# Optimization experiments

Hardware: AMD Instinct MI355X
Metric: run time of the kernel (lower is better)

The kernel has to match this reference:

```python
import jax, jax.numpy as jnp
import numpy as np

EPS = 1e-5

def knn_idx(x, k):
    # x: (B,C,N). Returns (B,N,k) indices of k nearest neighbors (by L2).
    inner = -2.0 * jnp.einsum('bcn,bcm->bnm', x, x)          # (B,N,N)
    xx = jnp.sum(x * x, axis=1)                               # (B,N)
    neg_dist = -xx[:, :, None] - inner - xx[:, None, :]       # (B,N,N)
    _, idx = jax.lax.top_k(neg_dist, k)                       # (B,N,k)
    return idx

def get_graph_features(x, k):
    # x: (B,C,N) -> (B,2C,N,k) with channels = concat(neighbor-center, center)
    B, C, N = x.shape
    idx = knn_idx(x, k)                                       # (B,N,k)
    pts = jnp.transpose(x, (0, 2, 1))                         # (B,N,C)
    nbr = jax.vmap(lambda p, i: p[i])(pts, idx)               # (B,N,k,C)
    ctr = jnp.broadcast_to(pts[:, :, None, :], nbr.shape)     # (B,N,k,C)
    feat = jnp.concatenate([nbr - ctr, ctr], axis=-1)         # (B,N,k,2C)
    return jnp.transpose(feat, (0, 3, 1, 2))                  # (B,2C,N,k)

def conv_bn_relu(y, W, gamma, beta):
    # 1x1 conv (pointwise matmul) + train-mode BatchNorm2d + ReLU
    y = jnp.einsum('oc,bcnk->bonk', W, y)
    mean = jnp.mean(y, axis=(0, 2, 3), keepdims=True)
    var = jnp.var(y, axis=(0, 2, 3), keepdims=True)
    yhat = (y - mean) * jax.lax.rsqrt(var + EPS)
    return jax.nn.relu(yhat * gamma[None, :, None, None] + beta[None, :, None, None])

def setup_inputs() -> dict:
    key = jax.random.key(0)
    ks = jax.random.split(key, 16)
    B, N, k, emb = 8, 2048, 20, 512
    x = jax.random.normal(ks[0], (B, 3, N), dtype=jnp.float32)
    def w(kk, o, c):
        return jax.random.normal(kk, (o, c), dtype=jnp.float32) * (1.0 / np.sqrt(c))
    inp = {
        'x': x, 'k': k,
        'W1': w(ks[1], 64, 6),   'W2': w(ks[2], 64, 64),
        'W3': w(ks[3], 128, 64), 'W4': w(ks[4], 256, 128),
        'W5': w(ks[5], emb, 512),
    }
    for i, c in zip(range(1, 6), [64, 64, 128, 256, emb]):
        inp[f'g{i}'] = 1.0 + 0.1 * jax.random.normal(ks[5 + i], (c,), dtype=jnp.float32)
        inp[f'b{i}'] = 0.1 * jax.random.normal(ks[10 + i], (c,), dtype=jnp.float32)
    return inp

def reference(x, W1, W2, W3, W4, W5, g1, b1, g2, b2, g3, b3, g4, b4, g5, b5, k):
    B, C, N = x.shape
    h = get_graph_features(x, k)                  # (B,6,N,k)
    h = conv_bn_relu(h, W1, g1, b1)               # (B,64,N,k)
    x1 = jnp.max(h, axis=-1, keepdims=True)
    h = conv_bn_relu(h, W2, g2, b2)               # (B,64,N,k)
    x2 = jnp.max(h, axis=-1, keepdims=True)
    h = conv_bn_relu(h, W3, g3, b3)               # (B,128,N,k)
    x3 = jnp.max(h, axis=-1, keepdims=True)
    h = conv_bn_relu(h, W4, g4, b4)               # (B,256,N,k)
    x4 = jnp.max(h, axis=-1, keepdims=True)
    cat = jnp.concatenate([x1, x2, x3, x4], axis=1)  # (B,512,N,1)
    out = conv_bn_relu(cat, W5, g5, b5)              # (B,emb,N,1)
    return out.reshape(B, -1, N)
```

## Files before the change

### kernel.cpp

```cpp
#include <hip/hip_runtime.h>
#include <hip/hip_bf16.h>

typedef __hip_bfloat16 bf16;
typedef __attribute__((ext_vector_type(8))) short short8v;
typedef __attribute__((ext_vector_type(4))) float f32x4;
typedef unsigned int uint;

#define BATCH 8
#define NPTS 2048
#define KNN 20
#define NK (NPTS*KNN)
#define P4 (BATCH*NK)
#define BN_TOT (BATCH*NPTS)

union BU { bf16 h; unsigned short u; };
__device__ __forceinline__ unsigned short f2bf(float f){
    BU bu; bu.h = __float2bfloat16(f); return bu.u;
}
__device__ __forceinline__ float bfu2f(unsigned short u){
    return __uint_as_float(((uint)u) << 16);
}

__global__ void initK(float* __restrict__ shadow)
{
    int t = blockIdx.x*256 + threadIdx.x;
    if (t < 5*16*1024) shadow[t] = 0.f;
}

__global__ void cvtWS(const float* __restrict__ src, short* __restrict__ dst, int Cin)
{
    int t = blockIdx.x*256 + threadIdx.x;
    int co = t / Cin, ci = t - co*Cin;
    dst[(size_t)co*Cin + (ci ^ ((co & 7) << 3))] = (short)f2bf(src[t]);
}

__global__ __launch_bounds__(256)
void knn_kernel(const float* __restrict__ x, int* __restrict__ idx)
{
    #pragma clang fp contract(off)
    __shared__ float sx[3*NPTS];
    __shared__ float sxx[NPTS];
    const int b  = blockIdx.x / (NPTS/4);
    const int nb = blockIdx.x % (NPTS/4);
    const float* xb = x + (size_t)b*3*NPTS;
    for (int i = threadIdx.x; i < 3*NPTS; i += 256) sx[i] = xb[i];
    __syncthreads();
    for (int i = threadIdx.x; i < NPTS; i += 256) {
        float y0 = sx[i], y1 = sx[NPTS+i], y2 = sx[2*NPTS+i];
        sxx[i] = y0*y0 + y1*y1 + y2*y2;
    }
    __syncthreads();

    const int wave = threadIdx.x >> 6;
    const int lane = threadIdx.x & 63;
    const int n = nb*4 + wave;

    const float x0 = sx[n], x1 = sx[NPTS+n], x2 = sx[2*NPTS+n];
    const float xxn = sxx[n];

    constexpr int L = 6;
    float best[L]; int bi[L];
    #pragma unroll
    for (int i = 0; i < L; ++i) { best[i] = -3e38f; bi[i] = 0x7fffffff; }

    #pragma unroll
    for (int j = 0; j < NPTS/64; ++j) {
        int m = lane + j*64;
        float dot = x0*sx[m] + x1*sx[NPTS+m] + x2*sx[2*NPTS+m];
        float v = -xxn - (-2.f*dot) - sxx[m];
        int mi = m;
        #pragma unroll
        for (int i = 0; i < L; ++i) {
            bool sw = v > best[i];
            float tv = sw ? best[i] : v;
            int   ti = sw ? bi[i]   : mi;
            best[i] = sw ? v  : best[i];
            bi[i]   = sw ? mi : bi[i];
            v = tv; mi = ti;
        }
    }

    size_t obase = ((size_t)b*NPTS + n)*KNN;
    int popped = 0;
    #pragma unroll 1
    for (int s = 0; s < KNN; ++s) {
        float mv = best[0]; int mi = bi[0];
        #pragma unroll
        for (int off = 1; off < 64; off <<= 1) {
            float ov = __shfl_xor(mv, off);
            int   oi = __shfl_xor(mi, off);
            if (ov > mv || (ov == mv && oi < mi)) { mv = ov; mi = oi; }
        }
        bool win = (best[0] == mv) && (bi[0] == mi);
        #pragma unroll
        for (int i = 0; i < L-1; ++i) {
            best[i] = win ? best[i+1] : best[i];
            bi[i]   = win ? bi[i+1]   : bi[i];
        }
        best[L-1] = win ? -3e38f     : best[L-1];
        bi[L-1]   = win ? 0x7fffffff : bi[L-1];
        popped += win ? 1 : 0;
        if (lane == 0) idx[obase + s] = mi;
    }

    if (__any(popped >= L)) {
        float B[KNN]; int BI[KNN];
        #pragma unroll
        for (int i = 0; i < KNN; ++i) { B[i] = -3e38f; BI[i] = 0x7fffffff; }
        #pragma unroll 1
        for (int j = 0; j < NPTS/64; ++j) {
            int m = lane + j*64;
            float dot = x0*sx[m] + x1*sx[NPTS+m] + x2*sx[2*NPTS+m];
            float v = -xxn - (-2.f*dot) - sxx[m];
            int mi = m;
            #pragma unroll
            for (int i = 0; i < KNN; ++i) {
                bool sw = v > B[i];
                float tv = sw ? B[i]  : v;
                int   ti = sw ? BI[i] : mi;
                B[i]  = sw ? v  : B[i];
                BI[i] = sw ? mi : BI[i];
                v = tv; mi = ti;
            }
        }
        #pragma unroll 1
        for (int s = 0; s < KNN; ++s) {
            float mv = B[0]; int mi = BI[0];
            #pragma unroll
            for (int off = 1; off < 64; off <<= 1) {
                float ov = __shfl_xor(mv, off);
                int   oi = __shfl_xor(mi, off);
                if (ov > mv || (ov == mv && oi < mi)) { mv = ov; mi = oi; }
            }
            bool win = (B[0] == mv) && (BI[0] == mi);
            #pragma unroll
            for (int i = 0; i < KNN-1; ++i) {
                B[i]  = win ? B[i+1]  : B[i];
                BI[i] = win ? BI[i+1] : BI[i];
            }
            B[KNN-1]  = win ? -3e38f     : B[KNN-1];
            BI[KNN-1] = win ? 0x7fffffff : BI[KNN-1];
            if (lane == 0) idx[obase + s] = mi;
        }
    }
}

__global__ void conv1T(const float* __restrict__ x, const int* __restrict__ idx,
                       const float* __restrict__ W1, bf16* __restrict__ h1)
{
    int p = blockIdx.x*256 + threadIdx.x;
    int b = p / NK;
    int r = p - b*NK;
    int n = r / KNN;
    int j = idx[p];
    const float* xb = x + (size_t)b*3*NPTS;
    float c0 = xb[n], c1 = xb[NPTS+n], c2 = xb[2*NPTS+n];
    float d0 = xb[j]-c0, d1 = xb[NPTS+j]-c1, d2 = xb[2*NPTS+j]-c2;
    uint4* outp = reinterpret_cast<uint4*>(reinterpret_cast<unsigned short*>(h1) + (size_t)p*64);
    #pragma unroll
    for (int ch = 0; ch < 8; ++ch) {
        uint u[4];
        #pragma unroll
        for (int q = 0; q < 4; ++q) {
            const float* wa = W1 + (ch*8 + q*2)*6;
            float a0 = wa[0]*d0 + wa[1]*d1 + wa[2]*d2 + wa[3]*c0 + wa[4]*c1 + wa[5]*c2;
            const float* wb = wa + 6;
            float a1 = wb[0]*d0 + wb[1]*d1 + wb[2]*d2 + wb[3]*c0 + wb[4]*c1 + wb[5]*c2;
            u[q] = (uint)f2bf(a0) | ((uint)f2bf(a1) << 16);
        }
        outp[ch] = make_uint4(u[0], u[1], u[2], u[3]);
    }
}

__global__ void statsT64(const bf16* __restrict__ h, float* __restrict__ shadow)
{
    __shared__ float ls[4][64], lq[4][64];
    int t = threadIdx.x;
    int c = t & 63, grp = t >> 6;
    const unsigned short* hp = reinterpret_cast<const unsigned short*>(h);
    size_t base = (size_t)blockIdx.x*1024;
    float s = 0.f, q = 0.f;
    for (int it = 0; it < 256; ++it) {
        size_t br = base + grp + (size_t)it*4;
        float v = bfu2f(hp[br*64 + c]);
        s += v; q += v*v;
    }
    ls[grp][c] = s; lq[grp][c] = q;
    __syncthreads();
    if (t < 64) {
        float S = ls[0][t]+ls[1][t]+ls[2][t]+ls[3][t];
        float Q = lq[0][t]+lq[1][t]+lq[2][t]+lq[3][t];
        float* sh = shadow + (size_t)(blockIdx.x & 15)*1024;
        atomicAdd(&sh[t], S);
        atomicAdd(&sh[512 + t], Q);
    }
}

__global__ void fin_kernel(const float* __restrict__ shadow,
                           const float* __restrict__ gamma, const float* __restrict__ beta,
                           float* __restrict__ scbiF, int C, float invCnt)
{
    for (int c = threadIdx.x; c < C; c += 256) {
        float s = 0.f, q = 0.f;
        #pragma unroll
        for (int i = 0; i < 16; ++i) { s += shadow[i*1024 + c]; q += shadow[i*1024 + 512 + c]; }
        float m = s*invCnt;
        float var = q*invCnt - m*m;
        float rs = rsqrtf(var + 1e-5f);
        float sc = rs * gamma[c];
        float bi = fmaf(-m, sc, beta[c]);
        scbiF[2*c] = sc; scbiF[2*c+1] = bi;
    }
}

template<int Cout, int Cin, int M, int POOL, int NSPLIT, int KTILE, int BT, int PF>
__global__ __launch_bounds__(BT)
void gemmT(const short* __restrict__ Wb, const bf16* __restrict__ in,
           bf16* __restrict__ outT, float* __restrict__ shadow,
           float* __restrict__ pmax, float* __restrict__ pmin)
{
    constexpr int CSPL = Cout/NSPLIT;
    constexpr int NT   = CSPL/16;
    constexpr int ROWS = (BT/64)*16*M;
    constexpr int KSTOT = Cin/32;
    constexpr int KPT   = KTILE/32;
    constexpr int NTILE = Cin/KTILE;
    constexpr size_t WB = (size_t)CSPL*KTILE*2;
    constexpr size_t PB = POOL ? (size_t)2*ROWS*17*4 : 0;
    constexpr size_t SB = WB > PB ? WB : PB;

    __shared__ __align__(16) char smem[SB];
    short* WsmS = reinterpret_cast<short*>(smem);
    float* poolF = reinterpret_cast<float*>(smem);

    const int tid  = threadIdx.x;
    const int lane = tid & 63;
    const int g = lane >> 4, mr = lane & 15;
    const int wid = tid >> 6;
    const int rowBlk = blockIdx.x*ROWS;
    const int rowW   = rowBlk + wid*(16*M);
    const int ntBase = blockIdx.y*CSPL;
    const short* inS = reinterpret_cast<const short*>(in);

    f32x4 acc[M][NT];
    #pragma unroll
    for (int m = 0; m < M; ++m)
    #pragma unroll
    for (int i = 0; i < NT; ++i) acc[m][i] = (f32x4){0.f,0.f,0.f,0.f};

    short8v a[M], anext[M];
    if (PF) {
        #pragma unroll
        for (int m = 0; m < M; ++m)
            a[m] = *reinterpret_cast<const short8v*>(inS + (size_t)(rowW + m*16 + mr)*Cin + 8*g);
    }

    #pragma unroll 1
    for (int kt = 0; kt < NTILE; ++kt) {
        if (kt) __syncthreads();
        {
            const int ktBase = kt*KTILE;
            for (int f8 = tid; f8 < CSPL*KTILE/8; f8 += BT) {
                int f = f8*8;
                int row = f / KTILE, col = f - row*KTILE;
                short8v v = *reinterpret_cast<const short8v*>(
                    Wb + (size_t)(ntBase + row)*Cin + ktBase + col);
                *reinterpret_cast<short8v*>(WsmS + f) = v;
            }
        }
        __syncthreads();

        #pragma unroll
        for (int ksl = 0; ksl < KPT; ++ksl) {
            const int ksg = kt*KPT + ksl;
            const int k0 = ksg*32 + 8*g;
            if (!PF) {
                #pragma unroll
                for (int m = 0; m < M; ++m)
                    a[m] = *reinterpret_cast<const short8v*>(inS + (size_t)(rowW + m*16 + mr)*Cin + k0);
            } else if (ksg + 1 < KSTOT) {
                #pragma unroll
                for (int m = 0; m < M; ++m)
                    anext[m] = *reinterpret_cast<const short8v*>(inS + (size_t)(rowW + m*16 + mr)*Cin + k0 + 32);
            }
            const int kx = ksl*32 + 8*g;
            #pragma unroll
            for (int nt = 0; nt < NT; ++nt) {
                const int brow = nt*16 + mr;
                short8v bfr = *reinterpret_cast<const short8v*>(
                    WsmS + brow*KTILE + (kx ^ ((mr & 7) << 3)));
                #pragma unroll
                for (int m = 0; m < M; ++m)
                    acc[m][nt] = __builtin_amdgcn_mfma_f32_16x16x32_bf16(a[m], bfr, acc[m][nt], 0, 0, 0);
            }
            if (PF) {
                #pragma unroll
                for (int m = 0; m < M; ++m) a[m] = anext[m];
            }
        }
    }

    float* sh = shadow + (size_t)((blockIdx.x ^ blockIdx.y) & 15)*1024;
    #pragma unroll
    for (int nt = 0; nt < NT; ++nt) {
        float s = 0.f, q = 0.f;
        #pragma unroll
        for (int m = 0; m < M; ++m)
        #pragma unroll
        for (int j = 0; j < 4; ++j) { float v = acc[m][nt][j]; s += v; q += v*v; }
        s += __shfl_xor(s, 16); s += __shfl_xor(s, 32);
        q += __shfl_xor(q, 16); q += __shfl_xor(q, 32);
        if (g == 0) {
            atomicAdd(&sh[ntBase + nt*16 + mr], s);
            atomicAdd(&sh[512 + ntBase + nt*16 + mr], q);
        }
    }

    if (!POOL) {
        #pragma unroll
        for (int m = 0; m < M; ++m)
        #pragma unroll
        for (int nt = 0; nt < NT; ++nt)
        #pragma unroll
        for (int j = 0; j < 4; ++j) {
            size_t row = (size_t)rowW + m*16 + g*4 + j;
            outT[row*Cout + ntBase + nt*16 + mr] = __float2bfloat16(acc[m][nt][j]);
        }
    } else {
        __syncthreads();
        #pragma unroll
        for (int np = 0; np < NT/2; ++np) {
            #pragma unroll
            for (int hh = 0; hh < 2; ++hh) {
                #pragma unroll
                for (int m = 0; m < M; ++m)
                #pragma unroll
                for (int j = 0; j < 4; ++j) {
                    int row = wid*(16*M) + m*16 + g*4 + j;
                    poolF[hh*(ROWS*17) + row*17 + mr] = acc[m][np*2+hh][j];
                }
            }
            __syncthreads();
            if (tid < 2*(ROWS/KNN)*16) {
                int hh = tid >> 7;
                int gg = (tid >> 4) & 7;
                int cc = tid & 15;
                float mx = -3e38f, mn = 3e38f;
                #pragma unroll
                for (int kk = 0; kk < KNN; ++kk) {
                    float v = poolF[hh*(ROWS*17) + (gg*KNN + kk)*17 + cc];
                    mx = fmaxf(mx, v); mn = fminf(mn, v);
                }
                int grp = rowBlk/KNN + gg;
                int c = ntBase + (np*2 + hh)*16 + cc;
                pmax[(size_t)grp*256 + c] = mx;
                pmin[(size_t)grp*256 + c] = mn;
            }
            __syncthreads();
        }
    }
}

template<int C>
__global__ void maxpoolT(bf16* __restrict__ h, const float* __restrict__ scbiF,
                         bf16* __restrict__ catT, int coff)
{
    constexpr int PB = 256/C;
    int t = threadIdx.x;
    int c = t & (C-1);
    int bn = blockIdx.x*PB + t/C;
    float sc = scbiF[2*c], bi = scbiF[2*c+1];
    unsigned short* src = reinterpret_cast<unsigned short*>(h) + (size_t)bn*KNN*C + c;
    float best = 0.f;
    #pragma unroll
    for (int kk = 0; kk < KNN; ++kk) {
        float a = fmaxf(fmaf(bfu2f(src[kk*C]), sc, bi), 0.f);
        src[kk*C] = f2bf(a);
        best = fmaxf(best, a);
    }
    catT[(size_t)bn*512 + coff + c] = __float2bfloat16(best);
}

__global__ void cat4T(const float* __restrict__ pmax, const float* __restrict__ pmin,
                      const float* __restrict__ scbiF, const float* __restrict__ g4,
                      bf16* __restrict__ catT)
{
    int t = blockIdx.x*256 + threadIdx.x;
    int c = t & 255, bn = t >> 8;
    float sc = scbiF[2*c], bi = scbiF[2*c+1];
    float v = (g4[c] >= 0.f) ? pmax[t] : pmin[t];
    catT[(size_t)bn*512 + 256 + c] = __float2bfloat16(fmaxf(fmaf(v, sc, bi), 0.f));
}

__global__ void finalT(const bf16* __restrict__ h5, const float* __restrict__ scbiF,
                       float* __restrict__ out)
{
    __shared__ float ls[64][65];
    int t = threadIdx.x;
    int b = blockIdx.z, n0 = blockIdx.x*64, c0 = blockIdx.y*64;
    int j = t & 63, i0 = t >> 6;
    float sc = scbiF[2*(c0+j)], bi = scbiF[2*(c0+j)+1];
    const unsigned short* hp = reinterpret_cast<const unsigned short*>(h5);
    for (int it = 0; it < 16; ++it) {
        int i = i0 + it*4;
        float v = bfu2f(hp[((size_t)(b*NPTS + n0 + i))*512 + c0 + j]);
        ls[i][j] = fmaxf(fmaf(v, sc, bi), 0.f);
    }
    __syncthreads();
    for (int it = 0; it < 16; ++it) {
        int cr = i0 + it*4;
        out[((size_t)b*512 + c0 + cr)*NPTS + n0 + j] = ls[j][cr];
    }
}

extern "C" void kernel_launch(void* const* d_in, const int* in_sizes, int n_in,
                              void* d_out, int out_size, void* d_ws, size_t ws_size,
                              hipStream_t stream)
{
    const float* x  = (const float*)d_in[0];
    const float* W1 = (const float*)d_in[2];
    const float* W2 = (const float*)d_in[3];
    const float* W3 = (const float*)d_in[4];
    const float* W4 = (const float*)d_in[5];
    const float* W5 = (const float*)d_in[6];
    const float* g1 = (const float*)d_in[7];  const float* b1 = (const float*)d_in[8];
    const float* g2 = (const float*)d_in[9];  const float* b2 = (const float*)d_in[10];
    const float* g3 = (const float*)d_in[11]; const float* b3 = (const float*)d_in[12];
    const float* g4 = (const float*)d_in[13]; const float* b4 = (const float*)d_in[14];
    const float* g5 = (const float*)d_in[15]; const float* b5 = (const float*)d_in[16];
    float* out = (float*)d_out;

    char* w = (char*)d_ws;
    int*   idx    = (int*)w;
    float* scbiF  = (float*)(w + 1323008);
    float* shadow = (float*)(w + 1343488);
    short* Wb     = (short*)(w + 1671168);
    bf16*  h1     = (bf16*)(w + 2285568);
    float* pmax   = (float*)h1;
    float* pmin   = pmax + (size_t)BN_TOT*256;
    bf16*  h2     = (bf16*)(w + 44228608);
    bf16*  h5     = h2;
    bf16*  h3     = (bf16*)(w + 86171648);
    bf16*  catT   = (bf16*)(w + 170057728);

    short* Wb2 = Wb, *Wb3 = Wb + 4096, *Wb4 = Wb + 12288, *Wb5 = Wb + 45056;
    float* sh1 = shadow, *sh2 = shadow + 16384, *sh3 = shadow + 2*16384,
         * sh4 = shadow + 3*16384, *sh5 = shadow + 4*16384;

    initK<<<320, 256, 0, stream>>>(shadow);
    cvtWS<<<16,   256, 0, stream>>>(W2, Wb2, 64);
    cvtWS<<<32,   256, 0, stream>>>(W3, Wb3, 64);
    cvtWS<<<128,  256, 0, stream>>>(W4, Wb4, 128);
    cvtWS<<<1024, 256, 0, stream>>>(W5, Wb5, 512);

    knn_kernel<<<BATCH*NPTS/4, 256, 0, stream>>>(x, idx);
    conv1T<<<P4/256, 256, 0, stream>>>(x, idx, W1, h1);

    statsT64<<<320, 256, 0, stream>>>(h1, sh1);
    fin_kernel<<<1, 256, 0, stream>>>(sh1, g1, b1, scbiF, 64, 1.f/P4);
    maxpoolT<64><<<BN_TOT/4, 256, 0, stream>>>(h1, scbiF, catT, 0);

    gemmT<64,64,2,0,1,64,256,1><<<dim3(P4/128,1), 256, 0, stream>>>(
        Wb2, h1, h2, sh2, nullptr, nullptr);
    fin_kernel<<<1, 256, 0, stream>>>(sh2, g2, b2, scbiF + 1024, 64, 1.f/P4);
    maxpoolT<64><<<BN_TOT/4, 256, 0, stream>>>(h2, scbiF + 1024, catT, 64);

    gemmT<128,64,2,0,2,64,256,1><<<dim3(P4/128,2), 256, 0, stream>>>(
        Wb3, h2, h3, sh3, nullptr, nullptr);
    fin_kernel<<<1, 256, 0, stream>>>(sh3, g3, b3, scbiF + 2048, 128, 1.f/P4);
    maxpoolT<128><<<BN_TOT/2, 256, 0, stream>>>(h3, scbiF + 2048, catT, 128);

    gemmT<256,128,2,1,2,128,320,1><<<dim3(P4/160,2), 320, 0, stream>>>(
        Wb4, h3, nullptr, sh4, pmax, pmin);
    fin_kernel<<<1, 256, 0, stream>>>(sh4, g4, b4, scbiF + 3072, 256, 1.f/P4);
    cat4T<<<BN_TOT, 256, 0, stream>>>(pmax, pmin, scbiF + 3072, g4, catT);

    gemmT<512,512,2,0,8,128,256,1><<<dim3(BN_TOT/128,8), 256, 0, stream>>>(
        Wb5, catT, h5, sh5, nullptr, nullptr);
    fin_kernel<<<1, 256, 0, stream>>>(sh5, g5, b5, scbiF + 4096, 512, 1.f/BN_TOT);
    finalT<<<dim3(NPTS/64, 8, BATCH), 256, 0, stream>>>(h5, scbiF + 4096, out);
}
```

Measured before the change: 392.9 us.

## Restructure kNN with packed float4 points, dual short lists, and 64-bit key reduction

The kNN kernel now stores each point as a float4 holding its coordinates and squared norm, so each candidate needs one LDS load. Each lane keeps two interleaved 4-entry insertion lists instead of one 6-entry list, which shortens the dependency chains. The 20 rounds of wave reduction shuffle a single packed 64-bit key (ordered float bits plus inverted index) instead of separate value and index. Blocks grow to 512 threads covering 8 query points, and two GEMM launches change how many output-channel tiles run per block in the grid's y dimension. Shorter per-lane lists make the slow full 20-entry fallback pass more likely to trigger.

```diff
diff --git a/kernel.cpp b/kernel.cpp
--- a/kernel.cpp
+++ b/kernel.cpp
@@ -5,6 +5,7 @@
 typedef __attribute__((ext_vector_type(8))) short short8v;
 typedef __attribute__((ext_vector_type(4))) float f32x4;
 typedef unsigned int uint;
+typedef unsigned long long u64;
 
 #define BATCH 8
 #define NPTS 2048
@@ -20,6 +21,10 @@
 __device__ __forceinline__ float bfu2f(unsigned short u){
     return __uint_as_float(((uint)u) << 16);
 }
+__device__ __forceinline__ uint fenc(float f){
+    uint b = __float_as_uint(f);
+    return (b & 0x80000000u) ? ~b : (b | 0x80000000u);
+}
 
 __global__ void initK(float* __restrict__ shadow)
 {
@@ -34,84 +39,99 @@
     dst[(size_t)co*Cin + (ci ^ ((co & 7) << 3))] = (short)f2bf(src[t]);
 }
 
-__global__ __launch_bounds__(256)
+__global__ __launch_bounds__(512)
 void knn_kernel(const float* __restrict__ x, int* __restrict__ idx)
 {
     #pragma clang fp contract(off)
-    __shared__ float sx[3*NPTS];
-    __shared__ float sxx[NPTS];
-    const int b  = blockIdx.x / (NPTS/4);
-    const int nb = blockIdx.x % (NPTS/4);
+    __shared__ float4 sp[NPTS];
+    const int b  = blockIdx.x / (NPTS/8);
+    const int nb = blockIdx.x % (NPTS/8);
     const float* xb = x + (size_t)b*3*NPTS;
-    for (int i = threadIdx.x; i < 3*NPTS; i += 256) sx[i] = xb[i];
-    __syncthreads();
-    for (int i = threadIdx.x; i < NPTS; i += 256) {
-        float y0 = sx[i], y1 = sx[NPTS+i], y2 = sx[2*NPTS+i];
-        sxx[i] = y0*y0 + y1*y1 + y2*y2;
+    for (int i = threadIdx.x; i < NPTS; i += 512) {
+        float y0 = xb[i], y1 = xb[NPTS+i], y2 = xb[2*NPTS+i];
+        float4 p; p.x = y0; p.y = y1; p.z = y2;
+        p.w = y0*y0 + y1*y1 + y2*y2;
+        sp[i] = p;
     }
     __syncthreads();
 
     const int wave = threadIdx.x >> 6;
     const int lane = threadIdx.x & 63;
-    const int n = nb*4 + wave;
-
-    const float x0 = sx[n], x1 = sx[NPTS+n], x2 = sx[2*NPTS+n];
-    const float xxn = sxx[n];
-
-    constexpr int L = 6;
-    float best[L]; int bi[L];
-    #pragma unroll
-    for (int i = 0; i < L; ++i) { best[i] = -3e38f; bi[i] = 0x7fffffff; }
-
-    #pragma unroll
-    for (int j = 0; j < NPTS/64; ++j) {
-        int m = lane + j*64;
-        float dot = x0*sx[m] + x1*sx[NPTS+m] + x2*sx[2*NPTS+m];
-        float v = -xxn - (-2.f*dot) - sxx[m];
-        int mi = m;
+    const int n = nb*8 + wave;
+
+    const float4 pn = sp[n];
+    const float x0 = pn.x, x1 = pn.y, x2 = pn.z;
+    const float xxn = pn.w;
+
+    constexpr int L = 4;
+    float bA[L], bB[L]; int iA[L], iB[L];
+    #pragma unroll
+    for (int i = 0; i < L; ++i) {
+        bA[i] = -3e38f; bB[i] = -3e38f; iA[i] = 0x7fffffff; iB[i] = 0x7fffffff;
+    }
+
+    #pragma unroll
+    for (int t = 0; t < NPTS/128; ++t) {
+        int m0 = lane + (2*t)*64, m1 = m0 + 64;
+        float4 p0 = sp[m0], p1 = sp[m1];
+        float dot0 = x0*p0.x + x1*p0.y + x2*p0.z;
+        float v0 = -xxn - (-2.f*dot0) - p0.w;
+        float dot1 = x0*p1.x + x1*p1.y + x2*p1.z;
+        float v1 = -xxn - (-2.f*dot1) - p1.w;
+        int mi0 = m0, mi1 = m1;
         #pragma unroll
         for (int i = 0; i < L; ++i) {
-            bool sw = v > best[i];
-            float tv = sw ? best[i] : v;
-            int   ti = sw ? bi[i]   : mi;
-            best[i] = sw ? v  : best[i];
-            bi[i]   = sw ? mi : bi[i];
-            v = tv; mi = ti;
-        }
+            { bool sw = v0 > bA[i];
+              float tv = sw ? bA[i] : v0; int ti = sw ? iA[i] : mi0;
+              bA[i] = sw ? v0 : bA[i]; iA[i] = sw ? mi0 : iA[i]; v0 = tv; mi0 = ti; }
+            { bool sw = v1 > bB[i];
+              float tv = sw ? bB[i] : v1; int ti = sw ? iB[i] : mi1;
+              bB[i] = sw ? v1 : bB[i]; iB[i] = sw ? mi1 : iB[i]; v1 = tv; mi1 = ti; }
+        }
+    }
+
+    u64 kA[L], kB[L];
+    #pragma unroll
+    for (int i = 0; i < L; ++i) {
+        kA[i] = ((u64)fenc(bA[i]) << 32) | (uint)(~iA[i]);
+        kB[i] = ((u64)fenc(bB[i]) << 32) | (uint)(~iB[i]);
     }
 
     size_t obase = ((size_t)b*NPTS + n)*KNN;
-    int popped = 0;
+    int popA = 0, popB = 0;
     #pragma unroll 1
     for (int s = 0; s < KNN; ++s) {
-        float mv = best[0]; int mi = bi[0];
+        bool useA = kA[0] >= kB[0];
+        u64 my = useA ? kA[0] : kB[0];
+        u64 g = my;
         #pragma unroll
         for (int off = 1; off < 64; off <<= 1) {
-            float ov = __shfl_xor(mv, off);
-            int   oi = __shfl_xor(mi, off);
-            if (ov > mv || (ov == mv && oi < mi)) { mv = ov; mi = oi; }
-        }
-        bool win = (best[0] == mv) && (bi[0] == mi);
+            u64 o = __shfl_xor(g, off);
+            g = (o > g) ? o : g;
+        }
+        if (lane == 0) idx[obase + s] = (int)(~(uint)g);
+        bool win = (my == g);
+        bool pA = win && useA, pB = win && !useA;
         #pragma unroll
         for (int i = 0; i < L-1; ++i) {
-            best[i] = win ? best[i+1] : best[i];
-            bi[i]   = win ? bi[i+1]   : bi[i];
-        }
-        best[L-1] = win ? -3e38f     : best[L-1];
-        bi[L-1]   = win ? 0x7fffffff : bi[L-1];
-        popped += win ? 1 : 0;
-        if (lane == 0) idx[obase + s] = mi;
-    }
-
-    if (__any(popped >= L)) {
+            kA[i] = pA ? kA[i+1] : kA[i];
+            kB[i] = pB ? kB[i+1] : kB[i];
+        }
+        kA[L-1] = pA ? 0ULL : kA[L-1];
+        kB[L-1] = pB ? 0ULL : kB[L-1];
+        popA += pA; popB += pB;
+    }
+
+    if (__any((popA >= L) || (popB >= L))) {
         float B[KNN]; int BI[KNN];
         #pragma unroll
         for (int i = 0; i < KNN; ++i) { B[i] = -3e38f; BI[i] = 0x7fffffff; }
         #pragma unroll 1
         for (int j = 0; j < NPTS/64; ++j) {
             int m = lane + j*64;
-            float dot = x0*sx[m] + x1*sx[NPTS+m] + x2*sx[2*NPTS+m];
-            float v = -xxn - (-2.f*dot) - sxx[m];
+            float4 p = sp[m];
+            float dot = x0*p.x + x1*p.y + x2*p.z;
+            float v = -xxn - (-2.f*dot) - p.w;
             int mi = m;
             #pragma unroll
             for (int i = 0; i < KNN; ++i) {
@@ -453,7 +473,7 @@
     cvtWS<<<128,  256, 0, stream>>>(W4, Wb4, 128);
     cvtWS<<<1024, 256, 0, stream>>>(W5, Wb5, 512);
 
-    knn_kernel<<<BATCH*NPTS/4, 256, 0, stream>>>(x, idx);
+    knn_kernel<<<BATCH*NPTS/8, 512, 0, stream>>>(x, idx);
     conv1T<<<P4/256, 256, 0, stream>>>(x, idx, W1, h1);
 
     statsT64<<<320, 256, 0, stream>>>(h1, sh1);
@@ -465,7 +485,7 @@
     fin_kernel<<<1, 256, 0, stream>>>(sh2, g2, b2, scbiF + 1024, 64, 1.f/P4);
     maxpoolT<64><<<BN_TOT/4, 256, 0, stream>>>(h2, scbiF + 1024, catT, 64);
 
-    gemmT<128,64,2,0,2,64,256,1><<<dim3(P4/128,2), 256, 0, stream>>>(
+    gemmT<128,64,2,0,1,64,256,1><<<dim3(P4/128,1), 256, 0, stream>>>(
         Wb3, h2, h3, sh3, nullptr, nullptr);
     fin_kernel<<<1, 256, 0, stream>>>(sh3, g3, b3, scbiF + 2048, 128, 1.f/P4);
     maxpoolT<128><<<BN_TOT/2, 256, 0, stream>>>(h3, scbiF + 2048, catT, 128);
@@ -475,7 +495,7 @@
     fin_kernel<<<1, 256, 0, stream>>>(sh4, g4, b4, scbiF + 3072, 256, 1.f/P4);
     cat4T<<<BN_TOT, 256, 0, stream>>>(pmax, pmin, scbiF + 3072, g4, catT);
 
-    gemmT<512,512,2,0,8,128,256,1><<<dim3(BN_TOT/128,8), 256, 0, stream>>>(
+    gemmT<512,512,2,0,4,128,256,1><<<dim3(BN_TOT/128,4), 256, 0, stream>>>(
         Wb5, catT, h5, sh5, nullptr, nullptr);
     fin_kernel<<<1, 256, 0, stream>>>(sh5, g5, b5, scbiF + 4096, 512, 1.f/BN_TOT);
     finalT<<<dim3(NPTS/64, 8, BATCH), 256, 0, stream>>>(h5, scbiF + 4096, out);
```

Measured after the change: 375.2 us. 4.5% less time.
